# Kernel tuning notes

Measured on AMD Instinct MI355X. Metric: run time of the kernel, lower is better.

The kernel has to match this reference:

```python
import jax, jax.numpy as jnp
import numpy as np

N = 4_194_304
H = 20
P = 10.0
MOMENTUM = 0.1


def setup_inputs() -> dict:
    key = jax.random.key(0)
    ks = jax.random.split(key, 12)
    w = 0.01  # init window from initialize_optimizer_params
    inp = {
        "grad_t": jax.random.normal(ks[0], (N, 1), dtype=jnp.float32),
        "loss_t": jnp.full((N, 1), 1.2345, dtype=jnp.float32),  # scalar loss broadcast
        "f_tm1": jnp.ones((N, 1), dtype=jnp.float32),
        "i_tm1": jnp.zeros((N, 1), dtype=jnp.float32),
        "theta_tm1": jax.random.normal(ks[1], (N, 1), dtype=jnp.float32) * np.sqrt(2.0 / N).astype(np.float32),
        "delta_tm1": jnp.zeros((N, 1), dtype=jnp.float32),
        "h0": jnp.zeros((N, H), dtype=jnp.float32),
        "c0": jnp.zeros((N, H), dtype=jnp.float32),
        "W_ih": jax.random.uniform(ks[2], (4 * H, 4), jnp.float32, -w, w),
        "W_hh": jax.random.uniform(ks[3], (4 * H, H), jnp.float32, -w, w),
        "b_ih": jax.random.uniform(ks[4], (4 * H,), jnp.float32, -w, w),
        "b_hh": jax.random.uniform(ks[5], (4 * H,), jnp.float32, -w, w),
        "W_theta_w": jax.random.uniform(ks[6], (1, H + 2), jnp.float32, -w, w),
        "W_theta_b": jax.random.uniform(ks[7], (1,), jnp.float32, 4.0, 5.0),
        "W_grad_w": jax.random.uniform(ks[8], (1, H + 2), jnp.float32, -w, w),
        "W_grad_b": jax.random.uniform(ks[9], (1,), jnp.float32, -5.0, -4.0),
    }
    return inp


def _preprocess(x):
    # x: [N]; returns [N, 2] with (log|x|/p or -1, sign(x) or x*e^p)
    eps = np.exp(-P).astype(np.float32)
    big = np.exp(P).astype(np.float32)
    ax = jnp.abs(x)
    cond = ax >= eps
    safe = jnp.where(cond, ax, 1.0)
    z1 = jnp.where(cond, jnp.log(safe) / P, -1.0)
    z2 = jnp.where(cond, jnp.sign(x), x * big)
    return jnp.stack([z1, z2], axis=-1)


def reference(grad_t, loss_t, f_tm1, i_tm1, theta_tm1, delta_tm1, h0, c0,
              W_ih, W_hh, b_ih, b_hh, W_theta_w, W_theta_b, W_grad_w, W_grad_b):
    # LSTM input: concat(preprocess(grad), preprocess(loss)) -> [N, 4]
    x = jnp.concatenate([_preprocess(grad_t[:, 0]), _preprocess(loss_t[:, 0])], axis=-1)
    # single LSTM step (PyTorch gate order i, f, g, o)
    gates = x @ W_ih.T + h0 @ W_hh.T + (b_ih + b_hh)  # [N, 4H]
    ig, fg, gg, og = jnp.split(gates, 4, axis=-1)
    ig = jax.nn.sigmoid(ig)
    fg = jax.nn.sigmoid(fg)
    gg = jnp.tanh(gg)
    og = jax.nn.sigmoid(og)
    c_t = fg * c0 + ig * gg
    h_t = og * jnp.tanh(c_t)  # [N, H] == output_t
    # gating heads: Linear(H+2 -> 1) + sigmoid
    f_in = jnp.concatenate([h_t, theta_tm1, f_tm1], axis=-1)  # [N, H+2]
    i_in = jnp.concatenate([h_t, theta_tm1, i_tm1], axis=-1)
    f_t = jax.nn.sigmoid(f_in @ W_theta_w.T + W_theta_b)  # [N, 1]
    i_t = jax.nn.sigmoid(i_in @ W_grad_w.T + W_grad_b)
    # gated momentum update
    delta_t = MOMENTUM * delta_tm1 - i_t * grad_t
    theta_t = f_t * theta_tm1 + delta_t
    return theta_t
```

## Files before the change

kernel.cpp:

```cpp
#include <hip/hip_runtime.h>

#define NP 16
#define WAVES 4
#define BLK (WAVES*64)

typedef __bf16 bf16x8 __attribute__((ext_vector_type(8)));
typedef float  f32x4  __attribute__((ext_vector_type(4)));

__device__ __forceinline__ float ex2(float x){ return __builtin_amdgcn_exp2f(x); }
__device__ __forceinline__ float rcp_(float x){ return __builtin_amdgcn_rcpf(x); }
__device__ __forceinline__ float lg2(float x){ return __builtin_amdgcn_logf(x); }
#define LOG2E 1.4426950408889634f

__device__ __forceinline__ float sigm(float x){ return rcp_(1.0f + ex2(-LOG2E*x)); }
__device__ __forceinline__ float tanh_(float x){ return 1.0f - 2.0f*rcp_(1.0f + ex2(2.8853900817779268f*x)); }

__device__ __forceinline__ unsigned cvtpk(float lo, float hi){
  unsigned r; asm("v_cvt_pk_bf16_f32 %0, %1, %2" : "=v"(r) : "v"(lo), "v"(hi)); return r;
}

__global__ __launch_bounds__(BLK) void lstm_opt_mfma(
    const float* __restrict__ grad, const float* __restrict__ loss,
    const float* __restrict__ f1,   const float* __restrict__ i1,
    const float* __restrict__ th1,  const float* __restrict__ dl1,
    const float* __restrict__ h0,   const float* __restrict__ c0,
    const float* __restrict__ Wih,  const float* __restrict__ Whh,
    const float* __restrict__ bih,  const float* __restrict__ bhh,
    const float* __restrict__ Wtw,  const float* __restrict__ Wtb,
    const float* __restrict__ Wgw,  const float* __restrict__ Wgb,
    float* __restrict__ out)
{
    const int tid  = threadIdx.x;
    const int lane = tid & 63;
    const int wid  = tid >> 6;
    const int e16  = lane & 15;
    const int grp  = lane >> 4;

    bf16x8 af[5];
    f32x4  bias4[5];
    float  wtwv[5], wgwv[5];
    int    jt[5];
    #pragma unroll
    for (int t = 0; t < 5; ++t) {
        const int gRow = t*16 + e16;
        const int j = gRow >> 2, gate = gRow & 3;
        const int r = gate*20 + j;
        float wf[8];
        #pragma unroll
        for (int i = 0; i < 8; ++i) {
            const int k = grp*8 + i;
            float v = 0.0f;
            if (k < 20)      v = Whh[r*20 + k];
            else if (k < 24) v = Wih[r*4 + (k - 20)];
            wf[i] = v;
        }
        union { unsigned u[4]; bf16x8 v; } pk;
        pk.u[0] = cvtpk(wf[0], wf[1]); pk.u[1] = cvtpk(wf[2], wf[3]);
        pk.u[2] = cvtpk(wf[4], wf[5]); pk.u[3] = cvtpk(wf[6], wf[7]);
        af[t] = pk.v;

        const int jj = 4*t + grp;
        jt[t] = jj;
        f32x4 b;
        #pragma unroll
        for (int m = 0; m < 4; ++m) b[m] = bih[m*20 + jj] + bhh[m*20 + jj];
        bias4[t] = b;
        wtwv[t] = Wtw[jj];
        wgwv[t] = Wgw[jj];
    }
    const float wt20 = Wtw[20], wt21 = Wtw[21], tb = Wtb[0];
    const float wg20 = Wgw[20], wg21 = Wgw[21], gb = Wgb[0];

    const int waveBase = (blockIdx.x * WAVES + wid) * (16 * NP);

    #pragma unroll 1
    for (int p = 0; p < NP; ++p) {
        const int e = waveBase + p*16 + e16;

        const float g  = grad[e];
        const float lv = loss[e];
        const float th = th1[e];
        const float ff = f1[e];
        const float ii = i1[e];
        const float dl = dl1[e];

        const float ax = fabsf(g);
        const bool  cg = ax >= 4.5399929762484854e-05f;
        const float x0 = cg ? lg2(ax) * 0.06931471805599453f : -1.0f;
        const float x1 = cg ? copysignf(1.0f, g) : g * 22026.465794806718f;
        const float al = fabsf(lv);
        const bool  cl = al >= 4.5399929762484854e-05f;
        const float x2 = cl ? lg2(al) * 0.06931471805599453f : -1.0f;
        const float x3 = cl ? copysignf(1.0f, lv) : lv * 22026.465794806718f;

        const float* hp = h0 + (size_t)e * 20;
        const int o0 = (grp == 0) ? 0 : (grp == 1) ? 8  : 16;
        const int o1 = (grp == 0) ? 4 : (grp == 1) ? 12 : 16;
        const float4 A4 = *(const float4*)(hp + o0);
        const float4 B4 = *(const float4*)(hp + o1);

        const bool z = (grp == 3);
        const float fa0 = z ? 0.0f : A4.x, fa1 = z ? 0.0f : A4.y;
        const float fa2 = z ? 0.0f : A4.z, fa3 = z ? 0.0f : A4.w;
        float fb0, fb1, fb2, fb3;
        if (grp == 2)      { fb0 = x0;  fb1 = x1;  fb2 = x2;  fb3 = x3;  }
        else if (z)        { fb0 = 0.f; fb1 = 0.f; fb2 = 0.f; fb3 = 0.f; }
        else               { fb0 = B4.x; fb1 = B4.y; fb2 = B4.z; fb3 = B4.w; }

        union { unsigned u[4]; bf16x8 v; } bp;
        bp.u[0] = cvtpk(fa0, fa1); bp.u[1] = cvtpk(fa2, fa3);
        bp.u[2] = cvtpk(fb0, fb1); bp.u[3] = cvtpk(fb2, fb3);
        const bf16x8 bfrag = bp.v;

        f32x4 acc[5];
        #pragma unroll
        for (int t = 0; t < 5; ++t) acc[t] = bias4[t];
        #pragma unroll
        for (int t = 0; t < 5; ++t)
            acc[t] = __builtin_amdgcn_mfma_f32_16x16x32_bf16(af[t], bfrag, acc[t], 0, 0, 0);

        float fac = 0.0f, iac = 0.0f;
        const float* cp = c0 + (size_t)e * 20;
        #pragma unroll
        for (int t = 0; t < 5; ++t) {
            const float c0v = cp[jt[t]];
            const float si = sigm(acc[t][0]);
            const float sf = sigm(acc[t][1]);
            const float tg = tanh_(acc[t][2]);
            const float so = sigm(acc[t][3]);
            const float ct = sf * c0v + si * tg;
            const float ht = so * tanh_(ct);
            fac += ht * wtwv[t];
            iac += ht * wgwv[t];
        }
        fac += __shfl_xor(fac, 16); fac += __shfl_xor(fac, 32);
        iac += __shfl_xor(iac, 16); iac += __shfl_xor(iac, 32);

        if (grp == 0) {
            const float ft = sigm(fac + tb + th*wt20 + ff*wt21);
            const float it = sigm(iac + gb + th*wg20 + ii*wg21);
            out[e] = ft*th + 0.1f*dl - it*g;
        }
    }
}

extern "C" void kernel_launch(void* const* d_in, const int* in_sizes, int n_in,
                              void* d_out, int out_size, void* d_ws, size_t ws_size,
                              hipStream_t stream) {
    const float* grad = (const float*)d_in[0];
    const float* loss = (const float*)d_in[1];
    const float* f1   = (const float*)d_in[2];
    const float* i1   = (const float*)d_in[3];
    const float* th1  = (const float*)d_in[4];
    const float* dl1  = (const float*)d_in[5];
    const float* h0   = (const float*)d_in[6];
    const float* c0   = (const float*)d_in[7];
    const float* Wih  = (const float*)d_in[8];
    const float* Whh  = (const float*)d_in[9];
    const float* bih  = (const float*)d_in[10];
    const float* bhh  = (const float*)d_in[11];
    const float* Wtw  = (const float*)d_in[12];
    const float* Wtb  = (const float*)d_in[13];
    const float* Wgw  = (const float*)d_in[14];
    const float* Wgb  = (const float*)d_in[15];

    const int N = in_sizes[0];
    const int blocks = N / (16 * NP * WAVES);
    hipLaunchKernelGGL(lstm_opt_mfma, dim3(blocks), dim3(BLK), 0, stream,
                       grad, loss, f1, i1, th1, dl1, h0, c0,
                       Wih, Whh, bih, bhh, Wtw, Wtb, Wgw, Wgb,
                       (float*)d_out);
}
```

Baseline: 220.8 us.

## Software-pipeline input loads, fold activation scales into weights, contiguous c0 access

Adds a double-buffered register prefetch so the grad, loss, h0 and c0 loads for the next chunk are issued before computing the current one, hiding global memory latency. Pre-multiplies the LSTM weights and biases by the exp2 scaling constants, and folds the 1/P log scale into W_ih, which removes per-element multiplies in the activations and preprocessing. Remaps hidden units so each lane group owns 5 contiguous c0 elements instead of strided ones. Also sets a launch-bounds occupancy hint; the cost is higher register pressure from holding two input sets at once.

```diff
diff --git a/kernel.cpp b/kernel.cpp
--- a/kernel.cpp
+++ b/kernel.cpp
@@ -10,16 +10,33 @@
 __device__ __forceinline__ float ex2(float x){ return __builtin_amdgcn_exp2f(x); }
 __device__ __forceinline__ float rcp_(float x){ return __builtin_amdgcn_rcpf(x); }
 __device__ __forceinline__ float lg2(float x){ return __builtin_amdgcn_logf(x); }
-#define LOG2E 1.4426950408889634f
-
-__device__ __forceinline__ float sigm(float x){ return rcp_(1.0f + ex2(-LOG2E*x)); }
-__device__ __forceinline__ float tanh_(float x){ return 1.0f - 2.0f*rcp_(1.0f + ex2(2.8853900817779268f*x)); }
-
-__device__ __forceinline__ unsigned cvtpk(float lo, float hi){
-  unsigned r; asm("v_cvt_pk_bf16_f32 %0, %1, %2" : "=v"(r) : "v"(lo), "v"(hi)); return r;
+
+#define LOG2E      1.4426950408889634f
+#define TWOLOG2E   2.8853900817779268f
+#define LN2_OVER_P 0.06931471805599453f
+#define NEG_PL2E  -14.426950408889634f
+#define EPSP       4.5399929762484854e-05f
+#define EXPP       22026.465794806718f
+
+struct InSet { float g, lv; float4 hA, hB; float c5[5]; };
+
+__device__ __forceinline__ void load_set(const float* __restrict__ grad,
+                                         const float* __restrict__ loss,
+                                         const float* __restrict__ h0,
+                                         const float* __restrict__ c0,
+                                         int e, int o0, int o1, int cOff, InSet& S)
+{
+    S.g  = grad[e];
+    S.lv = loss[e];
+    const float* hp = h0 + (size_t)e * 20;
+    S.hA = *(const float4*)(hp + o0);
+    S.hB = *(const float4*)(hp + o1);
+    const float* cp = c0 + (size_t)e * 20 + cOff;
+    #pragma unroll
+    for (int i = 0; i < 5; ++i) S.c5[i] = cp[i];
 }
 
-__global__ __launch_bounds__(BLK) void lstm_opt_mfma(
+__global__ __launch_bounds__(BLK, 4) void lstm_opt_mfma(
     const float* __restrict__ grad, const float* __restrict__ loss,
     const float* __restrict__ f1,   const float* __restrict__ i1,
     const float* __restrict__ th1,  const float* __restrict__ dl1,
@@ -39,97 +56,104 @@
     bf16x8 af[5];
     f32x4  bias4[5];
     float  wtwv[5], wgwv[5];
-    int    jt[5];
-    #pragma unroll
-    for (int t = 0; t < 5; ++t) {
-        const int gRow = t*16 + e16;
-        const int j = gRow >> 2, gate = gRow & 3;
-        const int r = gate*20 + j;
-        float wf[8];
+    {
+        const int gate = e16 & 3;
+        const int jA0  = 5 * (e16 >> 2);
+        const float sg = (gate == 2) ? TWOLOG2E : -LOG2E;
         #pragma unroll
-        for (int i = 0; i < 8; ++i) {
-            const int k = grp*8 + i;
-            float v = 0.0f;
-            if (k < 20)      v = Whh[r*20 + k];
-            else if (k < 24) v = Wih[r*4 + (k - 20)];
-            wf[i] = v;
-        }
-        union { unsigned u[4]; bf16x8 v; } pk;
-        pk.u[0] = cvtpk(wf[0], wf[1]); pk.u[1] = cvtpk(wf[2], wf[3]);
-        pk.u[2] = cvtpk(wf[4], wf[5]); pk.u[3] = cvtpk(wf[6], wf[7]);
-        af[t] = pk.v;
-
-        const int jj = 4*t + grp;
-        jt[t] = jj;
-        f32x4 b;
-        #pragma unroll
-        for (int m = 0; m < 4; ++m) b[m] = bih[m*20 + jj] + bhh[m*20 + jj];
-        bias4[t] = b;
-        wtwv[t] = Wtw[jj];
-        wgwv[t] = Wgw[jj];
+        for (int t = 0; t < 5; ++t) {
+            const int r = gate*20 + (jA0 + t);
+            float wf[8];
+            #pragma unroll
+            for (int i = 0; i < 8; ++i) {
+                const int k = grp*8 + i;
+                float v = 0.0f;
+                if (k < 20)      v = Whh[r*20 + k];
+                else if (k < 24) {
+                    v = Wih[r*4 + (k - 20)];
+                    if (k == 20 || k == 22) v *= LN2_OVER_P;
+                }
+                wf[i] = v * sg;
+            }
+            union { unsigned u[4]; bf16x8 v; } pk;
+            #pragma unroll
+            for (int q = 0; q < 4; ++q) {
+                unsigned r_;
+                asm("v_cvt_pk_bf16_f32 %0, %1, %2" : "=v"(r_) : "v"(wf[2*q]), "v"(wf[2*q+1]));
+                pk.u[q] = r_;
+            }
+            af[t] = pk.v;
+
+            const int jj = 5*grp + t;
+            f32x4 b;
+            #pragma unroll
+            for (int m = 0; m < 4; ++m) {
+                const float sm = (m == 2) ? TWOLOG2E : -LOG2E;
+                b[m] = (bih[m*20 + jj] + bhh[m*20 + jj]) * sm;
+            }
+            bias4[t] = b;
+            wtwv[t] = Wtw[jj];
+            wgwv[t] = Wgw[jj];
+        }
     }
     const float wt20 = Wtw[20], wt21 = Wtw[21], tb = Wtb[0];
     const float wg20 = Wgw[20], wg21 = Wgw[21], gb = Wgb[0];
 
+    const int o0   = (grp == 0) ? 0 : (grp == 1) ? 8  : 16;
+    const int o1   = (grp == 0) ? 4 : (grp == 1) ? 12 : 16;
+    const int cOff = 5 * grp;
     const int waveBase = (blockIdx.x * WAVES + wid) * (16 * NP);
 
-    #pragma unroll 1
-    for (int p = 0; p < NP; ++p) {
+    auto compute = [&](int p, const InSet& S) {
         const int e = waveBase + p*16 + e16;
-
-        const float g  = grad[e];
-        const float lv = loss[e];
         const float th = th1[e];
         const float ff = f1[e];
         const float ii = i1[e];
         const float dl = dl1[e];
 
+        const float g = S.g, lv = S.lv;
         const float ax = fabsf(g);
-        const bool  cg = ax >= 4.5399929762484854e-05f;
-        const float x0 = cg ? lg2(ax) * 0.06931471805599453f : -1.0f;
-        const float x1 = cg ? copysignf(1.0f, g) : g * 22026.465794806718f;
+        const bool  cg = ax >= EPSP;
+        const float u0 = cg ? lg2(ax) : NEG_PL2E;
+        const float x1 = cg ? copysignf(1.0f, g) : g * EXPP;
         const float al = fabsf(lv);
-        const bool  cl = al >= 4.5399929762484854e-05f;
-        const float x2 = cl ? lg2(al) * 0.06931471805599453f : -1.0f;
-        const float x3 = cl ? copysignf(1.0f, lv) : lv * 22026.465794806718f;
-
-        const float* hp = h0 + (size_t)e * 20;
-        const int o0 = (grp == 0) ? 0 : (grp == 1) ? 8  : 16;
-        const int o1 = (grp == 0) ? 4 : (grp == 1) ? 12 : 16;
-        const float4 A4 = *(const float4*)(hp + o0);
-        const float4 B4 = *(const float4*)(hp + o1);
+        const bool  cl = al >= EPSP;
+        const float u2 = cl ? lg2(al) : NEG_PL2E;
+        const float x3 = cl ? copysignf(1.0f, lv) : lv * EXPP;
 
         const bool z = (grp == 3);
-        const float fa0 = z ? 0.0f : A4.x, fa1 = z ? 0.0f : A4.y;
-        const float fa2 = z ? 0.0f : A4.z, fa3 = z ? 0.0f : A4.w;
+        const float fa0 = z ? 0.0f : S.hA.x, fa1 = z ? 0.0f : S.hA.y;
+        const float fa2 = z ? 0.0f : S.hA.z, fa3 = z ? 0.0f : S.hA.w;
         float fb0, fb1, fb2, fb3;
-        if (grp == 2)      { fb0 = x0;  fb1 = x1;  fb2 = x2;  fb3 = x3;  }
+        if (grp == 2)      { fb0 = u0;  fb1 = x1;  fb2 = u2;  fb3 = x3; }
         else if (z)        { fb0 = 0.f; fb1 = 0.f; fb2 = 0.f; fb3 = 0.f; }
-        else               { fb0 = B4.x; fb1 = B4.y; fb2 = B4.z; fb3 = B4.w; }
+        else               { fb0 = S.hB.x; fb1 = S.hB.y; fb2 = S.hB.z; fb3 = S.hB.w; }
 
         union { unsigned u[4]; bf16x8 v; } bp;
-        bp.u[0] = cvtpk(fa0, fa1); bp.u[1] = cvtpk(fa2, fa3);
-        bp.u[2] = cvtpk(fb0, fb1); bp.u[3] = cvtpk(fb2, fb3);
+        {
+            unsigned r0, r1, r2, r3;
+            asm("v_cvt_pk_bf16_f32 %0, %1, %2" : "=v"(r0) : "v"(fa0), "v"(fa1));
+            asm("v_cvt_pk_bf16_f32 %0, %1, %2" : "=v"(r1) : "v"(fa2), "v"(fa3));
+            asm("v_cvt_pk_bf16_f32 %0, %1, %2" : "=v"(r2) : "v"(fb0), "v"(fb1));
+            asm("v_cvt_pk_bf16_f32 %0, %1, %2" : "=v"(r3) : "v"(fb2), "v"(fb3));
+            bp.u[0] = r0; bp.u[1] = r1; bp.u[2] = r2; bp.u[3] = r3;
+        }
         const bf16x8 bfrag = bp.v;
 
         f32x4 acc[5];
         #pragma unroll
-        for (int t = 0; t < 5; ++t) acc[t] = bias4[t];
-        #pragma unroll
         for (int t = 0; t < 5; ++t)
-            acc[t] = __builtin_amdgcn_mfma_f32_16x16x32_bf16(af[t], bfrag, acc[t], 0, 0, 0);
+            acc[t] = __builtin_amdgcn_mfma_f32_16x16x32_bf16(af[t], bfrag, bias4[t], 0, 0, 0);
 
         float fac = 0.0f, iac = 0.0f;
-        const float* cp = c0 + (size_t)e * 20;
         #pragma unroll
         for (int t = 0; t < 5; ++t) {
-            const float c0v = cp[jt[t]];
-            const float si = sigm(acc[t][0]);
-            const float sf = sigm(acc[t][1]);
-            const float tg = tanh_(acc[t][2]);
-            const float so = sigm(acc[t][3]);
-            const float ct = sf * c0v + si * tg;
-            const float ht = so * tanh_(ct);
+            const float si = rcp_(1.0f + ex2(acc[t][0]));
+            const float sf = rcp_(1.0f + ex2(acc[t][1]));
+            const float tg = 1.0f - 2.0f * rcp_(1.0f + ex2(acc[t][2]));
+            const float so = rcp_(1.0f + ex2(acc[t][3]));
+            const float ct = sf * S.c5[t] + si * tg;
+            const float ht = so * (1.0f - 2.0f * rcp_(1.0f + ex2(TWOLOG2E * ct)));
             fac += ht * wtwv[t];
             iac += ht * wgwv[t];
         }
@@ -137,10 +161,21 @@
         iac += __shfl_xor(iac, 16); iac += __shfl_xor(iac, 32);
 
         if (grp == 0) {
-            const float ft = sigm(fac + tb + th*wt20 + ff*wt21);
-            const float it = sigm(iac + gb + th*wg20 + ii*wg21);
+            const float ft = rcp_(1.0f + ex2(-LOG2E * (fac + tb + th*wt20 + ff*wt21)));
+            const float it = rcp_(1.0f + ex2(-LOG2E * (iac + gb + th*wg20 + ii*wg21)));
             out[e] = ft*th + 0.1f*dl - it*g;
         }
+    };
+
+    InSet A, B;
+    load_set(grad, loss, h0, c0, waveBase + e16, o0, o1, cOff, A);
+    #pragma unroll 1
+    for (int p = 0; p < NP; p += 2) {
+        load_set(grad, loss, h0, c0, waveBase + (p+1)*16 + e16, o0, o1, cOff, B);
+        compute(p, A);
+        const int pn = (p + 2 < NP) ? (p + 2) : (NP - 1);
+        load_set(grad, loss, h0, c0, waveBase + pn*16 + e16, o0, o1, cOff, A);
+        compute(p + 1, B);
     }
 }
 
```

New measurement: 191.8 us. 1.15x faster.
